# Performance work log

Measured on AMD Instinct MI355X. Metric: run time of the kernel, lower is better.

Reference implementation:

```python
import jax, jax.numpy as jnp
import numpy as np

ATTN_HEADS = 4
NEG_INF = float(np.finfo(np.float32).min)


def setup_inputs() -> dict:
    key = jax.random.key(0)
    ks = jax.random.split(key, 7)
    B, N, K, Cin, Cout = 4, 4096, 32, 128, 128
    h_X = jax.random.normal(ks[0], (B, N, Cout), dtype=jnp.float32)
    h_E = jax.random.normal(ks[1], (B, N, K, Cin), dtype=jnp.float32)
    mask_attn = jax.random.randint(ks[2], (B, N, K), 0, 2, dtype=jnp.int32)
    # torch Linear weights are [out_features, in_features]
    W_Q = jax.random.normal(ks[3], (Cout, Cout), dtype=jnp.float32) / np.sqrt(Cout)
    W_K = jax.random.normal(ks[4], (Cout, Cin), dtype=jnp.float32) / np.sqrt(Cin)
    W_V = jax.random.normal(ks[5], (Cout, Cin), dtype=jnp.float32) / np.sqrt(Cin)
    W_O = jax.random.normal(ks[6], (Cout, 3 * Cout), dtype=jnp.float32) / np.sqrt(3 * Cout)
    return {"h_X": h_X, "h_E": h_E, "mask_attn": mask_attn,
            "W_Q": W_Q, "W_K": W_K, "W_V": W_V, "W_O": W_O}


def reference(h_X, h_E, mask_attn, W_Q, W_K, W_V, W_O):
    B, N, K, _ = h_E.shape
    C = W_Q.shape[0]
    H = ATTN_HEADS
    d = C // H

    h_q = (h_X @ W_Q.T).reshape(B, N, H, d)          # [B,N,H,d]
    h_k = (h_E @ W_K.T).reshape(B, N, K, H, d)       # [B,N,K,H,d]
    h_v = (h_E @ W_V.T).reshape(B, N, K, H, d)       # [B,N,K,H,d]

    # per-node, per-head scores over K neighbors
    scores = jnp.einsum('bnhd,bnkhd->bnhk', h_q, h_k) / np.sqrt(d)

    mask = (mask_attn[:, :, None, :] > 0)            # [B,N,1,K] -> broadcast over heads
    logits = jnp.where(mask, scores, NEG_INF)
    attn = jax.nn.softmax(logits, axis=-1) * mask.astype(scores.dtype)  # [B,N,H,K]

    attn_sum = attn.sum(axis=-1, keepdims=True) + 1e-8                  # [B,N,H,1]
    hv_t = jnp.swapaxes(h_v, 2, 3)                                      # [B,N,H,K,d]
    weighted_v = attn[..., None] * hv_t                                 # [B,N,H,K,d]
    weighted_sum = weighted_v.sum(axis=3)                               # [B,N,H,d]
    aggr_mean = (weighted_sum / attn_sum).reshape(B, N, C)
    aggr_sum = weighted_sum.reshape(B, N, C)
    aggr_max = weighted_v.max(axis=3).reshape(B, N, C)

    aggr_cat = jnp.concatenate([aggr_mean, aggr_sum, aggr_max], axis=-1)  # [B,N,3C]
    return aggr_cat @ W_O.T                                               # [B,N,C]
```

## Files before the change

### kernel.cpp

```cpp
#include <hip/hip_runtime.h>
#include <hip/hip_bf16.h>
#include <stdint.h>


typedef __attribute__((ext_vector_type(8))) short short8;
typedef __attribute__((ext_vector_type(4))) float f32x4;

#define NPB   16
#define CDIM  128
#define KN    32
#define ESTR  136
#define CATS  392
#define SSTR  36
#define NEGI  -3.0e38f

__device__ __forceinline__ float bf2f(short s) {
    union { unsigned int u; float f; } v;
    v.u = ((unsigned int)(unsigned short)s) << 16;
    return v.f;
}
__device__ __forceinline__ short f2bf(float f) {
    union { float ff; unsigned int u; } v; v.ff = f;
    unsigned int u = v.u;
    u += 0x7FFFu + ((u >> 16) & 1u);
    return (short)(u >> 16);
}

__device__ __forceinline__ short8 cvt8(const f32x4& a, const f32x4& b) {
    union { __hip_bfloat162 h; unsigned int u; } c0, c1, c2, c3;
    c0.h = __float22bfloat162_rn(float2{a[0], a[1]});
    c1.h = __float22bfloat162_rn(float2{a[2], a[3]});
    c2.h = __float22bfloat162_rn(float2{b[0], b[1]});
    c3.h = __float22bfloat162_rn(float2{b[2], b[3]});
    short8 r;
    r[0] = (short)(c0.u & 0xffff); r[1] = (short)(c0.u >> 16);
    r[2] = (short)(c1.u & 0xffff); r[3] = (short)(c1.u >> 16);
    r[4] = (short)(c2.u & 0xffff); r[5] = (short)(c2.u >> 16);
    r[6] = (short)(c3.u & 0xffff); r[7] = (short)(c3.u >> 16);
    return r;
}

template<bool FP32>
__device__ __forceinline__ short8 load8bf(const void* p, size_t idx) {
    if constexpr (FP32) {
        const float* fp = (const float*)p + idx;
        f32x4 a = *(const f32x4*)fp;
        f32x4 b = *(const f32x4*)(fp + 4);
        return cvt8(a, b);
    } else {
        return *(const short8*)((const short*)p + idx);
    }
}

template<bool FP32>
__device__ __forceinline__ short loadbf1(const void* p, size_t idx) {
    if constexpr (FP32) return f2bf(((const float*)p)[idx]);
    else return ((const short*)p)[idx];
}

__device__ __forceinline__ bool detect_fp32(const short* wp) {
    const int lane = threadIdx.x & 63;
    int cnt = 0;
    #pragma unroll
    for (int i = 0; i < 8; ++i) {
        const float v = bf2f(wp[lane + i * 64]);
        if (!(fabsf(v) < 8.0f)) cnt++;
    }
    #pragma unroll
    for (int d = 1; d < 64; d <<= 1) cnt += __shfl_xor(cnt, d);
    return cnt > 16;
}

struct alignas(16) Smem {
    short sE[128 * ESTR];
    short sT[64 * ESTR];
    short sQ[16 * ESTR];
    short sCat[16 * CATS];
    float sS[16 * SSTR];
    int   sMask[NPB * KN];
};

template<bool FP32>
__device__ __forceinline__ void issueE(const void* hE, size_t base, int tid,
                                       f32x4 (&eF)[8][2], short8 (&eB)[8]) {
    if constexpr (FP32) {
        #pragma unroll
        for (int it = 0; it < 8; ++it) {
            const float* p = (const float*)hE + base + (size_t)(it * 256 + tid) * 8;
            eF[it][0] = *(const f32x4*)p;
            eF[it][1] = *(const f32x4*)(p + 4);
        }
    } else {
        #pragma unroll
        for (int it = 0; it < 8; ++it)
            eB[it] = *(const short8*)((const short*)hE + base + (size_t)(it * 256 + tid) * 8);
    }
    __builtin_amdgcn_sched_barrier(0);
}

template<bool FP32>
__device__ __forceinline__ void writeE(short* sE, int tid,
                                       const f32x4 (&eF)[8][2], const short8 (&eB)[8]) {
    #pragma unroll
    for (int it = 0; it < 8; ++it) {
        const int chunk = it * 256 + tid, row = chunk >> 4, cc = chunk & 15;
        short8 v;
        if constexpr (FP32) v = cvt8(eF[it][0], eF[it][1]);
        else                v = eB[it];
        *(short8*)&sE[row * ESTR + cc * 8] = v;
    }
}

template<bool FP32>
__device__ __forceinline__ void na_body(Smem& sm,
    const void* __restrict__ hX, const void* __restrict__ hE,
    const int* __restrict__ mask, const void* __restrict__ WQ,
    const void* __restrict__ WK, const void* __restrict__ WV,
    const void* __restrict__ WO, void* __restrict__ out)
{
    const int tid  = threadIdx.x;
    const int lane = tid & 63;
    const int w    = tid >> 6;
    const int quad = lane >> 4;
    const int l15  = lane & 15;
    const int nb   = blockIdx.x * NPB;
    const size_t ebase = (size_t)nb * (KN * CDIM);

    f32x4 eF[8][2]; short8 eB[8];
    issueE<FP32>(hE, ebase, tid, eF, eB);

    *(int2*)&sm.sMask[tid * 2] = *(const int2*)&mask[(size_t)nb * KN + tid * 2];

    short8 ax[4];
    #pragma unroll
    for (int kk = 0; kk < 4; ++kk)
        ax[kk] = load8bf<FP32>(hX, (size_t)(nb + l15) * CDIM + kk * 32 + quad * 8);
    short8 bq[2][4];
    #pragma unroll
    for (int t2 = 0; t2 < 2; ++t2)
        #pragma unroll
        for (int kk = 0; kk < 4; ++kk)
            bq[t2][kk] = load8bf<FP32>(WQ, (size_t)(w * 32 + t2 * 16 + l15) * CDIM + kk * 32 + quad * 8);

    {
        f32x4 o0 = {0.f,0.f,0.f,0.f}, o1 = {0.f,0.f,0.f,0.f};
        #pragma unroll
        for (int kk = 0; kk < 4; ++kk) {
            o0 = __builtin_amdgcn_mfma_f32_16x16x32_bf16(ax[kk], bq[0][kk], o0, 0, 0, 0);
            o1 = __builtin_amdgcn_mfma_f32_16x16x32_bf16(ax[kk], bq[1][kk], o1, 0, 0, 0);
        }
        #pragma unroll
        for (int r = 0; r < 4; ++r) {
            const int n = quad * 4 + r;
            sm.sQ[n * ESTR + w * 32 + l15]      = f2bf(o0[r]);
            sm.sQ[n * ESTR + w * 32 + 16 + l15] = f2bf(o1[r]);
        }
    }
    __syncthreads();

    short8 bk[2][4];
    #pragma unroll
    for (int t2 = 0; t2 < 2; ++t2)
        #pragma unroll
        for (int kk = 0; kk < 4; ++kk) {
            const int j = w * 32 + t2 * 16 + l15;
            short8 b;
            #pragma unroll
            for (int jj = 0; jj < 8; ++jj)
                b[jj] = loadbf1<FP32>(WK, (size_t)(kk * 32 + quad * 8 + jj) * CDIM + j);
            bk[t2][kk] = b;
        }

    {
        const float scale = 0.17677669529663687f;
        const short8 zz = {0,0,0,0,0,0,0,0};
        #pragma unroll
        for (int m = 0; m < 4; ++m) {
            const int n_g = m * 4 + (l15 >> 2), h_ = l15 & 3;
            const short8 qv = *(const short8*)&sm.sQ[n_g * ESTR + h_ * 32 + quad * 8];
            f32x4 c0 = {0.f,0.f,0.f,0.f}, c1 = {0.f,0.f,0.f,0.f};
            #pragma unroll
            for (int kk = 0; kk < 4; ++kk) {
                const short8 af = (kk == h_) ? qv : zz;
                c0 = __builtin_amdgcn_mfma_f32_16x16x32_bf16(af, bk[0][kk], c0, 0, 0, 0);
                c1 = __builtin_amdgcn_mfma_f32_16x16x32_bf16(af, bk[1][kk], c1, 0, 0, 0);
            }
            #pragma unroll
            for (int r = 0; r < 4; ++r) {
                const int row = m * 16 + quad * 4 + r;
                sm.sT[row * ESTR + w * 32 + l15]      = f2bf(c0[r] * scale);
                sm.sT[row * ESTR + w * 32 + 16 + l15] = f2bf(c1[r] * scale);
            }
        }
    }

    short8 bv[2][4];
    #pragma unroll
    for (int ct2 = 0; ct2 < 2; ++ct2)
        #pragma unroll
        for (int kk = 0; kk < 4; ++kk)
            bv[ct2][kk] = load8bf<FP32>(WV, (size_t)((2 * w + ct2) * 16 + l15) * CDIM + kk * 32 + quad * 8);

    writeE<FP32>(sm.sE, tid, eF, eB);
    issueE<FP32>(hE, ebase + 1 * 128 * 128, tid, eF, eB);
    __syncthreads();

    #pragma unroll 1
    for (int s = 0; s < 4; ++s) {
        short8 bs[4], a0[4], a1[4];
        #pragma unroll
        for (int kk = 0; kk < 4; ++kk) {
            bs[kk] = *(const short8*)&sm.sT[(16 * s + l15) * ESTR + kk * 32 + quad * 8];
            a0[kk] = *(const short8*)&sm.sE[(w * 32 + l15) * ESTR + kk * 32 + quad * 8];
            a1[kk] = *(const short8*)&sm.sE[(w * 32 + 16 + l15) * ESTR + kk * 32 + quad * 8];
        }
        f32x4 s0 = {0.f,0.f,0.f,0.f}, s1 = {0.f,0.f,0.f,0.f};
        #pragma unroll
        for (int kk = 0; kk < 4; ++kk) {
            s0 = __builtin_amdgcn_mfma_f32_16x16x32_bf16(a0[kk], bs[kk], s0, 0, 0, 0);
            s1 = __builtin_amdgcn_mfma_f32_16x16x32_bf16(a1[kk], bs[kk], s1, 0, 0, 0);
        }

        {
            const int* mp = &sm.sMask[(s * 4 + (l15 >> 2)) * KN];
            float x[8]; int mk[8];
            #pragma unroll
            for (int j = 0; j < 4; ++j) {
                x[j] = s0[j];     mk[j]     = mp[quad * 4 + j];
                x[4 + j] = s1[j]; mk[4 + j] = mp[16 + quad * 4 + j];
            }
            float m = NEGI;
            #pragma unroll
            for (int j = 0; j < 8; ++j) m = fmaxf(m, (mk[j] > 0) ? x[j] : NEGI);
            m = fmaxf(m, __shfl_xor(m, 16));
            m = fmaxf(m, __shfl_xor(m, 32));
            float dsum = 0.f;
            #pragma unroll
            for (int j = 0; j < 8; ++j) {
                const float e = __expf(fminf(x[j] - m, 0.f)) * ((mk[j] > 0) ? 1.f : 0.f);
                x[j] = e; dsum += e;
            }
            dsum += __shfl_xor(dsum, 16);
            dsum += __shfl_xor(dsum, 32);
            const float inv = (dsum > 0.f) ? (1.f / dsum) : 0.f;
            if ((l15 >> 2) == w) {
                float* sp = &sm.sS[(w * 4 + (l15 & 3)) * SSTR];
                #pragma unroll
                for (int j = 0; j < 4; ++j) {
                    sp[quad * 4 + j]      = x[j] * inv;
                    sp[16 + quad * 4 + j] = x[4 + j] * inv;
                }
                if (quad == 0)
                    sp[33] = 1.0f / (((dsum > 0.f) ? 1.0f : 0.0f) + 1e-8f);
            }
        }
        __syncthreads();

        #pragma unroll
        for (int n_ = 0; n_ < 4; ++n_) {
            short8 c0[4], c1[4];
            #pragma unroll
            for (int kk = 0; kk < 4; ++kk) {
                c0[kk] = *(const short8*)&sm.sE[(n_ * 32 + l15) * ESTR + kk * 32 + quad * 8];
                c1[kk] = *(const short8*)&sm.sE[(n_ * 32 + 16 + l15) * ESTR + kk * 32 + quad * 8];
            }
            const float* ap = &sm.sS[(n_ * 4 + w) * SSTR];
            const float ainv = ap[33];
            #pragma unroll
            for (int ct2 = 0; ct2 < 2; ++ct2) {
                f32x4 av0 = {0.f,0.f,0.f,0.f}, av1 = {0.f,0.f,0.f,0.f};
                #pragma unroll
                for (int kk = 0; kk < 4; ++kk) {
                    av0 = __builtin_amdgcn_mfma_f32_16x16x32_bf16(c0[kk], bv[ct2][kk], av0, 0, 0, 0);
                    av1 = __builtin_amdgcn_mfma_f32_16x16x32_bf16(c1[kk], bv[ct2][kk], av1, 0, 0, 0);
                }
                float sum = 0.f, mx = NEGI;
                #pragma unroll
                for (int r = 0; r < 4; ++r) {
                    const float p0 = ap[quad * 4 + r]      * av0[r];
                    const float p1 = ap[16 + quad * 4 + r] * av1[r];
                    sum += p0 + p1;
                    mx = fmaxf(mx, fmaxf(p0, p1));
                }
                sum += __shfl_xor(sum, 16);
                sum += __shfl_xor(sum, 32);
                mx = fmaxf(mx, __shfl_xor(mx, 16));
                mx = fmaxf(mx, __shfl_xor(mx, 32));
                if (quad == 0) {
                    const int c = (2 * w + ct2) * 16 + l15, row = s * 4 + n_;
                    sm.sCat[row * CATS + c]       = f2bf(sum * ainv);
                    sm.sCat[row * CATS + 128 + c] = f2bf(sum);
                    sm.sCat[row * CATS + 256 + c] = f2bf(mx);
                }
            }
        }
        __syncthreads();

        if (s < 3) {
            writeE<FP32>(sm.sE, tid, eF, eB);
            if (s < 2) issueE<FP32>(hE, ebase + (size_t)(s + 2) * 128 * 128, tid, eF, eB);
            __syncthreads();
        }
    }

    {
        f32x4 o0 = {0.f,0.f,0.f,0.f}, o1 = {0.f,0.f,0.f,0.f};
        #pragma unroll
        for (int kk = 0; kk < 12; ++kk) {
            const short8 a  = *(const short8*)&sm.sCat[l15 * CATS + kk * 32 + quad * 8];
            const short8 b0 = load8bf<FP32>(WO, (size_t)(w * 32 + l15) * 384 + kk * 32 + quad * 8);
            const short8 b1 = load8bf<FP32>(WO, (size_t)(w * 32 + 16 + l15) * 384 + kk * 32 + quad * 8);
            o0 = __builtin_amdgcn_mfma_f32_16x16x32_bf16(a, b0, o0, 0, 0, 0);
            o1 = __builtin_amdgcn_mfma_f32_16x16x32_bf16(a, b1, o1, 0, 0, 0);
        }
        #pragma unroll
        for (int r = 0; r < 4; ++r) {
            const int node = quad * 4 + r;
            const size_t base = (size_t)(nb + node) * CDIM + w * 32;
            if constexpr (FP32) {
                ((float*)out)[base + l15]      = o0[r];
                ((float*)out)[base + 16 + l15] = o1[r];
            } else {
                ((short*)out)[base + l15]      = f2bf(o0[r]);
                ((short*)out)[base + 16 + l15] = f2bf(o1[r]);
            }
        }
    }
}

__global__ __launch_bounds__(256, 2)
void na_fused(const void* __restrict__ hX, const void* __restrict__ hE,
              const int* __restrict__ mask, const void* __restrict__ WQ,
              const void* __restrict__ WK, const void* __restrict__ WV,
              const void* __restrict__ WO, void* __restrict__ out)
{
    __shared__ Smem sm;
    if (detect_fp32((const short*)WQ)) na_body<true >(sm, hX, hE, mask, WQ, WK, WV, WO, out);
    else                               na_body<false>(sm, hX, hE, mask, WQ, WK, WV, WO, out);
}

extern "C" void kernel_launch(void* const* d_in, const int* in_sizes, int n_in,
                              void* d_out, int out_size, void* d_ws, size_t ws_size,
                              hipStream_t stream) {
    (void)in_sizes; (void)n_in; (void)ws_size; (void)out_size; (void)d_ws;
    const void* hX   = d_in[0];
    const void* hE   = d_in[1];
    const int*  mask = (const int*)d_in[2];
    const void* WQ   = d_in[3];
    const void* WK   = d_in[4];
    const void* WV   = d_in[5];
    const void* WO   = d_in[6];

    na_fused<<<dim3(1024), dim3(256), 0, stream>>>(hX, hE, mask, WQ, WK, WV, WO, d_out);
}
```

Measured before the change: 401.2 us.

## Process one node per iteration with double-buffered edge tiles and shuffle-based attention

The main loop now handles one node per iteration instead of four. Each node's 32x128 edge tile sits in a small double-buffered shared slot, and the next node's tile is prefetched while the current one is computed. Attention weights move between lanes through shuffles instead of a shared scratch array, which drops one barrier per step. The score A-fragments are reused for the value MFMAs, and sQ/sCat share a union, cutting shared memory enough to raise the occupancy target to 3 blocks. The trade-off is 16 barriers instead of about 8, smaller per-step load batches, and only one wave's work's worth of latency hiding per step.

```diff
diff --git a/kernel.cpp b/kernel.cpp
--- a/kernel.cpp
+++ b/kernel.cpp
@@ -11,7 +11,6 @@
 #define KN    32
 #define ESTR  136
 #define CATS  392
-#define SSTR  36
 #define NEGI  -3.0e38f
 
 __device__ __forceinline__ float bf2f(short s) {
@@ -72,42 +71,43 @@
 }
 
 struct alignas(16) Smem {
-    short sE[128 * ESTR];
+    short sEb[2][32 * ESTR];
     short sT[64 * ESTR];
-    short sQ[16 * ESTR];
-    short sCat[16 * CATS];
-    float sS[16 * SSTR];
+    union {
+        short sQ[16 * ESTR];
+        short sCat[16 * CATS];
+    } u;
     int   sMask[NPB * KN];
 };
 
 template<bool FP32>
-__device__ __forceinline__ void issueE(const void* hE, size_t base, int tid,
-                                       f32x4 (&eF)[8][2], short8 (&eB)[8]) {
+__device__ __forceinline__ void issueN(const void* hE, size_t base, int tid,
+                                       f32x4 (&pF)[2][2], short8 (&pB)[2]) {
     if constexpr (FP32) {
         #pragma unroll
-        for (int it = 0; it < 8; ++it) {
+        for (int it = 0; it < 2; ++it) {
             const float* p = (const float*)hE + base + (size_t)(it * 256 + tid) * 8;
-            eF[it][0] = *(const f32x4*)p;
-            eF[it][1] = *(const f32x4*)(p + 4);
+            pF[it][0] = *(const f32x4*)p;
+            pF[it][1] = *(const f32x4*)(p + 4);
         }
     } else {
         #pragma unroll
-        for (int it = 0; it < 8; ++it)
-            eB[it] = *(const short8*)((const short*)hE + base + (size_t)(it * 256 + tid) * 8);
+        for (int it = 0; it < 2; ++it)
+            pB[it] = *(const short8*)((const short*)hE + base + (size_t)(it * 256 + tid) * 8);
     }
     __builtin_amdgcn_sched_barrier(0);
 }
 
 template<bool FP32>
-__device__ __forceinline__ void writeE(short* sE, int tid,
-                                       const f32x4 (&eF)[8][2], const short8 (&eB)[8]) {
-    #pragma unroll
-    for (int it = 0; it < 8; ++it) {
+__device__ __forceinline__ void writeN(short* dst, int tid,
+                                       const f32x4 (&pF)[2][2], const short8 (&pB)[2]) {
+    #pragma unroll
+    for (int it = 0; it < 2; ++it) {
         const int chunk = it * 256 + tid, row = chunk >> 4, cc = chunk & 15;
         short8 v;
-        if constexpr (FP32) v = cvt8(eF[it][0], eF[it][1]);
-        else                v = eB[it];
-        *(short8*)&sE[row * ESTR + cc * 8] = v;
+        if constexpr (FP32) v = cvt8(pF[it][0], pF[it][1]);
+        else                v = pB[it];
+        *(short8*)&dst[row * ESTR + cc * 8] = v;
     }
 }
 
@@ -126,8 +126,8 @@
     const int nb   = blockIdx.x * NPB;
     const size_t ebase = (size_t)nb * (KN * CDIM);
 
-    f32x4 eF[8][2]; short8 eB[8];
-    issueE<FP32>(hE, ebase, tid, eF, eB);
+    f32x4 pF[2][2]; short8 pB[2];
+    issueN<FP32>(hE, ebase, tid, pF, pB);
 
     *(int2*)&sm.sMask[tid * 2] = *(const int2*)&mask[(size_t)nb * KN + tid * 2];
 
@@ -141,7 +141,6 @@
         #pragma unroll
         for (int kk = 0; kk < 4; ++kk)
             bq[t2][kk] = load8bf<FP32>(WQ, (size_t)(w * 32 + t2 * 16 + l15) * CDIM + kk * 32 + quad * 8);
-
     {
         f32x4 o0 = {0.f,0.f,0.f,0.f}, o1 = {0.f,0.f,0.f,0.f};
         #pragma unroll
@@ -152,8 +151,8 @@
         #pragma unroll
         for (int r = 0; r < 4; ++r) {
             const int n = quad * 4 + r;
-            sm.sQ[n * ESTR + w * 32 + l15]      = f2bf(o0[r]);
-            sm.sQ[n * ESTR + w * 32 + 16 + l15] = f2bf(o1[r]);
+            sm.u.sQ[n * ESTR + w * 32 + l15]      = f2bf(o0[r]);
+            sm.u.sQ[n * ESTR + w * 32 + 16 + l15] = f2bf(o1[r]);
         }
     }
     __syncthreads();
@@ -170,14 +169,13 @@
                 b[jj] = loadbf1<FP32>(WK, (size_t)(kk * 32 + quad * 8 + jj) * CDIM + j);
             bk[t2][kk] = b;
         }
-
     {
         const float scale = 0.17677669529663687f;
         const short8 zz = {0,0,0,0,0,0,0,0};
         #pragma unroll
         for (int m = 0; m < 4; ++m) {
             const int n_g = m * 4 + (l15 >> 2), h_ = l15 & 3;
-            const short8 qv = *(const short8*)&sm.sQ[n_g * ESTR + h_ * 32 + quad * 8];
+            const short8 qv = *(const short8*)&sm.u.sQ[n_g * ESTR + h_ * 32 + quad * 8];
             f32x4 c0 = {0.f,0.f,0.f,0.f}, c1 = {0.f,0.f,0.f,0.f};
             #pragma unroll
             for (int kk = 0; kk < 4; ++kk) {
@@ -201,19 +199,22 @@
         for (int kk = 0; kk < 4; ++kk)
             bv[ct2][kk] = load8bf<FP32>(WV, (size_t)((2 * w + ct2) * 16 + l15) * CDIM + kk * 32 + quad * 8);
 
-    writeE<FP32>(sm.sE, tid, eF, eB);
-    issueE<FP32>(hE, ebase + 1 * 128 * 128, tid, eF, eB);
+    writeN<FP32>(sm.sEb[0], tid, pF, pB);
+    issueN<FP32>(hE, ebase + 1 * (KN * CDIM), tid, pF, pB);
     __syncthreads();
 
     #pragma unroll 1
-    for (int s = 0; s < 4; ++s) {
-        short8 bs[4], a0[4], a1[4];
+    for (int i = 0; i < NPB; ++i) {
+        const short* bufp = sm.sEb[i & 1];
+
+        short8 a0[4], a1[4], bs[4];
         #pragma unroll
         for (int kk = 0; kk < 4; ++kk) {
-            bs[kk] = *(const short8*)&sm.sT[(16 * s + l15) * ESTR + kk * 32 + quad * 8];
-            a0[kk] = *(const short8*)&sm.sE[(w * 32 + l15) * ESTR + kk * 32 + quad * 8];
-            a1[kk] = *(const short8*)&sm.sE[(w * 32 + 16 + l15) * ESTR + kk * 32 + quad * 8];
-        }
+            bs[kk] = *(const short8*)&sm.sT[(i * 4 + (l15 & 3)) * ESTR + kk * 32 + quad * 8];
+            a0[kk] = *(const short8*)&bufp[l15 * ESTR + kk * 32 + quad * 8];
+            a1[kk] = *(const short8*)&bufp[(16 + l15) * ESTR + kk * 32 + quad * 8];
+        }
+
         f32x4 s0 = {0.f,0.f,0.f,0.f}, s1 = {0.f,0.f,0.f,0.f};
         #pragma unroll
         for (int kk = 0; kk < 4; ++kk) {
@@ -221,9 +222,10 @@
             s1 = __builtin_amdgcn_mfma_f32_16x16x32_bf16(a1[kk], bs[kk], s1, 0, 0, 0);
         }
 
+        float x[8], ainv;
         {
-            const int* mp = &sm.sMask[(s * 4 + (l15 >> 2)) * KN];
-            float x[8]; int mk[8];
+            const int* mp = &sm.sMask[i * KN];
+            int mk[8];
             #pragma unroll
             for (int j = 0; j < 4; ++j) {
                 x[j] = s0[j];     mk[j]     = mp[quad * 4 + j];
@@ -243,42 +245,39 @@
             dsum += __shfl_xor(dsum, 16);
             dsum += __shfl_xor(dsum, 32);
             const float inv = (dsum > 0.f) ? (1.f / dsum) : 0.f;
-            if ((l15 >> 2) == w) {
-                float* sp = &sm.sS[(w * 4 + (l15 & 3)) * SSTR];
-                #pragma unroll
-                for (int j = 0; j < 4; ++j) {
-                    sp[quad * 4 + j]      = x[j] * inv;
-                    sp[16 + quad * 4 + j] = x[4 + j] * inv;
-                }
-                if (quad == 0)
-                    sp[33] = 1.0f / (((dsum > 0.f) ? 1.0f : 0.0f) + 1e-8f);
-            }
-        }
-        __syncthreads();
-
-        #pragma unroll
-        for (int n_ = 0; n_ < 4; ++n_) {
-            short8 c0[4], c1[4];
-            #pragma unroll
-            for (int kk = 0; kk < 4; ++kk) {
-                c0[kk] = *(const short8*)&sm.sE[(n_ * 32 + l15) * ESTR + kk * 32 + quad * 8];
-                c1[kk] = *(const short8*)&sm.sE[(n_ * 32 + 16 + l15) * ESTR + kk * 32 + quad * 8];
-            }
-            const float* ap = &sm.sS[(n_ * 4 + w) * SSTR];
-            const float ainv = ap[33];
+            #pragma unroll
+            for (int j = 0; j < 8; ++j) x[j] *= inv;
+            ainv = 1.0f / (((dsum > 0.f) ? 1.0f : 0.0f) + 1e-8f);
+        }
+
+        if (i < NPB - 1) {
+            writeN<FP32>(sm.sEb[(i + 1) & 1], tid, pF, pB);
+            if (i < NPB - 2)
+                issueN<FP32>(hE, ebase + (size_t)(i + 2) * (KN * CDIM), tid, pF, pB);
+        }
+
+        {
+            const int src = (quad << 4) | w;
+            float aA[4], aB[4];
+            #pragma unroll
+            for (int r = 0; r < 4; ++r) {
+                aA[r] = __shfl(x[r], src);
+                aB[r] = __shfl(x[4 + r], src);
+            }
+            const float ainvw = __shfl(ainv, src);
             #pragma unroll
             for (int ct2 = 0; ct2 < 2; ++ct2) {
                 f32x4 av0 = {0.f,0.f,0.f,0.f}, av1 = {0.f,0.f,0.f,0.f};
                 #pragma unroll
                 for (int kk = 0; kk < 4; ++kk) {
-                    av0 = __builtin_amdgcn_mfma_f32_16x16x32_bf16(c0[kk], bv[ct2][kk], av0, 0, 0, 0);
-                    av1 = __builtin_amdgcn_mfma_f32_16x16x32_bf16(c1[kk], bv[ct2][kk], av1, 0, 0, 0);
+                    av0 = __builtin_amdgcn_mfma_f32_16x16x32_bf16(a0[kk], bv[ct2][kk], av0, 0, 0, 0);
+                    av1 = __builtin_amdgcn_mfma_f32_16x16x32_bf16(a1[kk], bv[ct2][kk], av1, 0, 0, 0);
                 }
                 float sum = 0.f, mx = NEGI;
                 #pragma unroll
                 for (int r = 0; r < 4; ++r) {
-                    const float p0 = ap[quad * 4 + r]      * av0[r];
-                    const float p1 = ap[16 + quad * 4 + r] * av1[r];
+                    const float p0 = aA[r] * av0[r];
+                    const float p1 = aB[r] * av1[r];
                     sum += p0 + p1;
                     mx = fmaxf(mx, fmaxf(p0, p1));
                 }
@@ -287,27 +286,21 @@
                 mx = fmaxf(mx, __shfl_xor(mx, 16));
                 mx = fmaxf(mx, __shfl_xor(mx, 32));
                 if (quad == 0) {
-                    const int c = (2 * w + ct2) * 16 + l15, row = s * 4 + n_;
-                    sm.sCat[row * CATS + c]       = f2bf(sum * ainv);
-                    sm.sCat[row * CATS + 128 + c] = f2bf(sum);
-                    sm.sCat[row * CATS + 256 + c] = f2bf(mx);
+                    const int c = (2 * w + ct2) * 16 + l15;
+                    sm.u.sCat[i * CATS + c]       = f2bf(sum * ainvw);
+                    sm.u.sCat[i * CATS + 128 + c] = f2bf(sum);
+                    sm.u.sCat[i * CATS + 256 + c] = f2bf(mx);
                 }
             }
         }
         __syncthreads();
-
-        if (s < 3) {
-            writeE<FP32>(sm.sE, tid, eF, eB);
-            if (s < 2) issueE<FP32>(hE, ebase + (size_t)(s + 2) * 128 * 128, tid, eF, eB);
-            __syncthreads();
-        }
     }
 
     {
         f32x4 o0 = {0.f,0.f,0.f,0.f}, o1 = {0.f,0.f,0.f,0.f};
         #pragma unroll
         for (int kk = 0; kk < 12; ++kk) {
-            const short8 a  = *(const short8*)&sm.sCat[l15 * CATS + kk * 32 + quad * 8];
+            const short8 a  = *(const short8*)&sm.u.sCat[l15 * CATS + kk * 32 + quad * 8];
             const short8 b0 = load8bf<FP32>(WO, (size_t)(w * 32 + l15) * 384 + kk * 32 + quad * 8);
             const short8 b1 = load8bf<FP32>(WO, (size_t)(w * 32 + 16 + l15) * 384 + kk * 32 + quad * 8);
             o0 = __builtin_amdgcn_mfma_f32_16x16x32_bf16(a, b0, o0, 0, 0, 0);
@@ -328,7 +321,7 @@
     }
 }
 
-__global__ __launch_bounds__(256, 2)
+__global__ __launch_bounds__(256, 3)
 void na_fused(const void* __restrict__ hX, const void* __restrict__ hE,
               const int* __restrict__ mask, const void* __restrict__ WQ,
               const void* __restrict__ WK, const void* __restrict__ WV,
```

Result: no change. 398.2 us (-0.8%).
